# Kernel tuning notes

Measured on AMD Instinct MI355X. Metric: run time of the kernel, lower is better.

## Reference

```python
import jax, jax.numpy as jnp
import numpy as np

D_MODEL = 1024
D_HIDDEN = 4096
NUM_EXPERTS = 8
TOP_K = 2
B, S = 2, 2048


def setup_inputs() -> dict:
    key = jax.random.key(0)
    ks = jax.random.split(key, 9)
    sc = 0.02
    x = jax.random.normal(ks[0], (B, S, D_MODEL), dtype=jnp.float32)
    w1 = jax.random.normal(ks[1], (NUM_EXPERTS, D_MODEL, D_HIDDEN), dtype=jnp.float32) * sc
    b1 = jnp.zeros((NUM_EXPERTS, D_HIDDEN), dtype=jnp.float32)
    w2 = jax.random.normal(ks[2], (NUM_EXPERTS, D_MODEL, D_HIDDEN), dtype=jnp.float32) * sc
    b2 = jnp.zeros((NUM_EXPERTS, D_HIDDEN), dtype=jnp.float32)
    wo = jax.random.normal(ks[3], (NUM_EXPERTS, D_HIDDEN, D_MODEL), dtype=jnp.float32) * sc
    bo = jnp.zeros((NUM_EXPERTS, D_MODEL), dtype=jnp.float32)
    router_w = jax.random.normal(ks[4], (D_MODEL, NUM_EXPERTS), dtype=jnp.float32) * sc
    router_b = jnp.zeros((NUM_EXPERTS,), dtype=jnp.float32)
    return {"x": x, "router_w": router_w, "router_b": router_b,
            "w1": w1, "b1": b1, "w2": w2, "b2": b2, "wo": wo, "bo": bo}


def reference(x, router_w, router_b, w1, b1, w2, b2, wo, bo):
    b, s, d = x.shape
    E = w1.shape[0]
    xf = x.reshape(-1, d)                               # [T, d]
    logits = xf @ router_w + router_b                   # [T, E]
    probs = jax.nn.softmax(logits, axis=-1)
    topk_p, topk_i = jax.lax.top_k(probs, TOP_K)        # [T, K]
    onehot = jax.nn.one_hot(topk_i, E, dtype=probs.dtype)  # [T, K, E]
    combine = (onehot * topk_p[..., None]).sum(axis=1)  # [T, E] per-token expert weight
    out = jnp.zeros_like(xf)
    for e in range(E):  # fixed small expert loop; weight is 0 for unselected tokens
        h = (xf @ w1[e] + b1[e]) * jax.nn.silu(xf @ w2[e] + b2[e])  # [T, H]
        out = out + combine[:, e:e + 1] * (h @ wo[e] + bo[e])
    # load-balancing loss: fraction of tokens routed to each expert x mean prob
    f_i = (onehot.sum(axis=1) > 0).astype(probs.dtype).mean(axis=0)  # [E]
    P_i = probs.mean(axis=0)                                          # [E]
    lb_loss = 0.01 * E * jnp.sum(f_i * P_i)
    return out.reshape(b, s, d), lb_loss
```

## Files before the change

kernel.cpp:

```cpp
#include <hip/hip_runtime.h>
#include <hip/hip_bf16.h>
#include <stdint.h>


#define T_TOKENS 4096
#define DM 1024
#define DH 4096
#define N_EXP 8
#define N_PAIRS (T_TOKENS * 2)
#define MAX_TILES 96

typedef __hip_bfloat16 bf16_t;
typedef __bf16 bf16x8 __attribute__((ext_vector_type(8)));
typedef float  f32x4  __attribute__((ext_vector_type(4)));
typedef unsigned short ushort4v __attribute__((ext_vector_type(4)));

#define WS_COUNTS   0
#define WS_OFFSETS  32
#define WS_PSUM     96
#define WS_NTILES   128
#define WS_CURSOR   192
#define WS_TILE_E   256
#define WS_TILE_M0  768
#define WS_E_OF     4096
#define WS_W_OF     69632
#define WS_TOK_OF   102400
#define WS_WT_OF    135168
#define WS_SLOT_OF  167936
#define WS_HBUF     (1u<<20)
#define WS_YPAIR    (WS_HBUF + (size_t)N_PAIRS*DH*2)
#define WS_NEEDED   (WS_YPAIR + (size_t)N_PAIRS*DM*2)
#define WS_XBF      WS_NEEDED
#define WS_W1T      (WS_XBF + (size_t)T_TOKENS*DM*2)
#define WS_W2T      (WS_W1T + (size_t)N_EXP*DM*DH*2)
#define WS_WOT      (WS_W2T + (size_t)N_EXP*DM*DH*2)
#define WS_NEEDED_BIG (WS_WOT + (size_t)N_EXP*DM*DH*2)

#define PITCH 40

__device__ __forceinline__ unsigned short f2bf(float f) {
  bf16_t h = __float2bfloat16(f);
  return *(unsigned short*)&h;
}

__device__ __forceinline__ void gload16(const void* g, void* l) {
  __builtin_amdgcn_global_load_lds(
      (const __attribute__((address_space(1))) unsigned int*)g,
      (__attribute__((address_space(3))) unsigned int*)l, 16, 0, 0);
}

#define RT_BLOCKS 64
#define RT_TPB (T_TOKENS / RT_BLOCKS)
#define RT_TPW (RT_TPB / 4)

__global__ __launch_bounds__(256) void k_router(const float* __restrict__ x,
                                                const float* __restrict__ rw,
                                                const float* __restrict__ rb,
                                                char* __restrict__ ws) {
  __shared__ float s_psum[4][8];
  __shared__ unsigned long long s_hist[4];
  int tid = threadIdx.x, lane = tid & 63, wave = tid >> 6;
  int t0 = blockIdx.x * RT_TPB + wave * RT_TPW;
  int* e_of = (int*)(ws + WS_E_OF);
  float* w_of = (float*)(ws + WS_W_OF);

  float lpsum[8];
#pragma unroll
  for (int e = 0; e < 8; ++e) lpsum[e] = 0.f;
  unsigned long long lhist = 0ull;

  for (int tt = 0; tt < RT_TPW; ++tt) {
    int t = t0 + tt;
    float acc[8];
#pragma unroll
    for (int e = 0; e < 8; ++e) acc[e] = 0.f;
    const float* xr = x + (size_t)t * DM;
    for (int j = lane; j < DM; j += 64) {
      float xv = xr[j];
      float4 r01 = *(const float4*)(rw + j * 8);
      float4 r23 = *(const float4*)(rw + j * 8 + 4);
      acc[0] += xv * r01.x; acc[1] += xv * r01.y;
      acc[2] += xv * r01.z; acc[3] += xv * r01.w;
      acc[4] += xv * r23.x; acc[5] += xv * r23.y;
      acc[6] += xv * r23.z; acc[7] += xv * r23.w;
    }
#pragma unroll
    for (int m = 1; m < 64; m <<= 1) {
#pragma unroll
      for (int e = 0; e < 8; ++e) acc[e] += __shfl_xor(acc[e], m);
    }
    float mx = -1e30f;
#pragma unroll
    for (int e = 0; e < 8; ++e) { acc[e] += rb[e]; mx = fmaxf(mx, acc[e]); }
    float s = 0.f;
#pragma unroll
    for (int e = 0; e < 8; ++e) { acc[e] = __expf(acc[e] - mx); s += acc[e]; }
    float inv = 1.f / s;
#pragma unroll
    for (int e = 0; e < 8; ++e) { acc[e] *= inv; lpsum[e] += acc[e]; }
    int i1 = 0;
#pragma unroll
    for (int e = 1; e < 8; ++e) if (acc[e] > acc[i1]) i1 = e;
    int i2 = -1;
#pragma unroll
    for (int e = 0; e < 8; ++e) if (e != i1 && (i2 < 0 || acc[e] > acc[i2])) i2 = e;
    lhist += (1ull << (i1 * 8)) + (1ull << (i2 * 8));
    if (lane == 0) {
      e_of[2 * t] = i1; e_of[2 * t + 1] = i2;
      w_of[2 * t] = acc[i1]; w_of[2 * t + 1] = acc[i2];
    }
  }
  if (lane == 0) {
#pragma unroll
    for (int e = 0; e < 8; ++e) s_psum[wave][e] = lpsum[e];
    s_hist[wave] = lhist;
  }
  __syncthreads();
  if (tid < 8) {
    float p = s_psum[0][tid] + s_psum[1][tid] + s_psum[2][tid] + s_psum[3][tid];
    atomicAdd((float*)(ws + WS_PSUM) + tid, p);
    int c = 0;
#pragma unroll
    for (int w = 0; w < 4; ++w) c += (int)((s_hist[w] >> (tid * 8)) & 0xff);
    atomicAdd((int*)(ws + WS_COUNTS) + tid, c);
  }
}

__global__ void k_scan(char* __restrict__ ws, float* __restrict__ out) {
  if (threadIdx.x == 0 && blockIdx.x == 0) {
    int* counts = (int*)(ws + WS_COUNTS);
    int* offs = (int*)(ws + WS_OFFSETS);
    int* te = (int*)(ws + WS_TILE_E);
    int* tm = (int*)(ws + WS_TILE_M0);
    int off = 0, nt = 0;
    for (int e = 0; e < 8; ++e) {
      offs[e] = off;
      for (int m0 = 0; m0 < counts[e]; m0 += 128) { te[nt] = e; tm[nt] = off + m0; ++nt; }
      off += counts[e];
    }
    *(int*)(ws + WS_NTILES) = nt;
    float* psum = (float*)(ws + WS_PSUM);
    float lb = 0.f;
    for (int e = 0; e < 8; ++e)
      lb += ((float)counts[e] / (float)T_TOKENS) * (psum[e] / (float)T_TOKENS);
    lb *= 0.01f * 8.f;
    out[(size_t)T_TOKENS * DM] = lb;
  }
}

__global__ __launch_bounds__(256) void k_fill(char* __restrict__ ws) {
  __shared__ int hist[8];
  __shared__ int base[8];
  int tid = threadIdx.x;
  int i = blockIdx.x * 256 + tid;
  if (tid < 8) hist[tid] = 0;
  __syncthreads();
  int e = ((const int*)(ws + WS_E_OF))[i];
  int rank = atomicAdd(&hist[e], 1);
  __syncthreads();
  if (tid < 8) base[tid] = atomicAdd((int*)(ws + WS_CURSOR) + tid, hist[tid]);
  __syncthreads();
  int slot = ((const int*)(ws + WS_OFFSETS))[e] + base[e] + rank;
  ((int*)(ws + WS_TOK_OF))[slot] = i >> 1;
  ((float*)(ws + WS_WT_OF))[slot] = ((const float*)(ws + WS_W_OF))[i];
  ((int*)(ws + WS_SLOT_OF))[i] = slot;
}

__global__ __launch_bounds__(256) void k_cvt_x(const float* __restrict__ x,
                                               char* __restrict__ ws) {
  int i = blockIdx.x * 256 + threadIdx.x;
  const float* s = x + (size_t)i * 8;
  float4 a = *(const float4*)s;
  float4 b = *(const float4*)(s + 4);
  uint4 v;
  v.x = (unsigned)f2bf(a.x) | ((unsigned)f2bf(a.y) << 16);
  v.y = (unsigned)f2bf(a.z) | ((unsigned)f2bf(a.w) << 16);
  v.z = (unsigned)f2bf(b.x) | ((unsigned)f2bf(b.y) << 16);
  v.w = (unsigned)f2bf(b.z) | ((unsigned)f2bf(b.w) << 16);
  *(uint4*)(ws + WS_XBF + (size_t)i * 16) = v;
}

__global__ __launch_bounds__(256) void k_transp(const float* __restrict__ in,
                                                char* __restrict__ outc,
                                                int K, int N) {
  __shared__ __align__(16) float tile[64][68];
  int e = blockIdx.z;
  int k0 = blockIdx.y * 64, n0 = blockIdx.x * 64;
  int tid = threadIdx.x;
  const float* src = in + ((size_t)e * K + k0) * N + n0;
  int row = tid >> 2, c4 = (tid & 3) * 16;
#pragma unroll
  for (int j = 0; j < 4; ++j)
    *(float4*)&tile[row][c4 + j * 4] = *(const float4*)(src + (size_t)row * N + c4 + j * 4);
  __syncthreads();
  int n = tid >> 2, kc = (tid & 3) * 16;
  unsigned int pk[8];
#pragma unroll
  for (int j = 0; j < 8; ++j) {
    unsigned int lo = f2bf(tile[kc + 2 * j][n]);
    unsigned int hi = f2bf(tile[kc + 2 * j + 1][n]);
    pk[j] = lo | (hi << 16);
  }
  char* dst = outc + ((size_t)e * K * N + (size_t)(n0 + n) * K + k0 + kc) * 2;
  uint4 v0 = {pk[0], pk[1], pk[2], pk[3]};
  uint4 v1 = {pk[4], pk[5], pk[6], pk[7]};
  *(uint4*)dst = v0;
  *(uint4*)(dst + 16) = v1;
}

__global__ __launch_bounds__(256, 2) void k_gemm1_bf(const float* __restrict__ b1,
                                                     const float* __restrict__ b2,
                                                     char* __restrict__ ws) {
  __shared__ __align__(16) unsigned short As[128 * 64];
  __shared__ __align__(16) unsigned short Bs1[64 * 64];
  __shared__ __align__(16) unsigned short Bs2[64 * 64];
  __shared__ int tokLds[128];
  int tid = threadIdx.x;
  int tileIdx = blockIdx.y;
  if (tileIdx >= *(const int*)(ws + WS_NTILES)) return;
  int e = ((const int*)(ws + WS_TILE_E))[tileIdx];
  int m_start = ((const int*)(ws + WS_TILE_M0))[tileIdx];
  int m_end = ((const int*)(ws + WS_OFFSETS))[e] + ((const int*)(ws + WS_COUNTS))[e];
  int m_cnt = min(128, m_end - m_start);
  int n0 = blockIdx.x * 64;
  if (tid < 128) tokLds[tid] = ((const int*)(ws + WS_TOK_OF))[m_start + min(tid, m_cnt - 1)];
  __syncthreads();

  int lane = tid & 63, wave = tid >> 6;
  int wm = wave >> 1, wn = wave & 1;
  int lr = lane & 15, quad = lane >> 4;
  int lsub = lane >> 3;
  int clog = (lane & 7) ^ lsub;

  const char* xbf = ws + WS_XBF;
  const char* w1t = ws + WS_W1T + (size_t)e * DM * DH * 2;
  const char* w2t = ws + WS_W2T + (size_t)e * DM * DH * 2;

  const char* srcA[4];
#pragma unroll
  for (int i = 0; i < 4; ++i) {
    int r = (wave * 4 + i) * 8 + lsub;
    srcA[i] = xbf + (size_t)tokLds[r] * (DM * 2) + clog * 16;
  }
  const char* srcB1[2];
  const char* srcB2[2];
#pragma unroll
  for (int i = 0; i < 2; ++i) {
    int r = (wave * 2 + i) * 8 + lsub;
    srcB1[i] = w1t + (size_t)(n0 + r) * (DM * 2) + clog * 16;
    srcB2[i] = w2t + (size_t)(n0 + r) * (DM * 2) + clog * 16;
  }

  f32x4 acc1[4][2], acc2[4][2];
  f32x4 z = {0.f, 0.f, 0.f, 0.f};
#pragma unroll
  for (int i = 0; i < 4; ++i)
#pragma unroll
    for (int j = 0; j < 2; ++j) { acc1[i][j] = z; acc2[i][j] = z; }

  for (int kt = 0; kt < DM / 64; ++kt) {
    int kb = kt * 128;
#pragma unroll
    for (int i = 0; i < 4; ++i)
      gload16(srcA[i] + kb, &As[(wave * 4 + i) * 512]);
#pragma unroll
    for (int i = 0; i < 2; ++i) {
      gload16(srcB1[i] + kb, &Bs1[(wave * 2 + i) * 512]);
      gload16(srcB2[i] + kb, &Bs2[(wave * 2 + i) * 512]);
    }
    __syncthreads();
#pragma unroll
    for (int s = 0; s < 2; ++s) {
      int sw = (((s * 4 + quad) ^ (lr & 7)) << 3);
      bf16x8 a[4], f1[2], f2v[2];
#pragma unroll
      for (int mt = 0; mt < 4; ++mt)
        a[mt] = *(const bf16x8*)&As[(wm * 64 + mt * 16 + lr) * 64 + sw];
#pragma unroll
      for (int nt = 0; nt < 2; ++nt) {
        int off = (wn * 32 + nt * 16 + lr) * 64 + sw;
        f1[nt]  = *(const bf16x8*)&Bs1[off];
        f2v[nt] = *(const bf16x8*)&Bs2[off];
      }
#pragma unroll
      for (int mt = 0; mt < 4; ++mt)
#pragma unroll
        for (int nt = 0; nt < 2; ++nt) {
          acc1[mt][nt] = __builtin_amdgcn_mfma_f32_16x16x32_bf16(a[mt], f1[nt],  acc1[mt][nt], 0, 0, 0);
          acc2[mt][nt] = __builtin_amdgcn_mfma_f32_16x16x32_bf16(a[mt], f2v[nt], acc2[mt][nt], 0, 0, 0);
        }
    }
    __syncthreads();
  }
  bf16_t* Hbuf = (bf16_t*)(ws + WS_HBUF);
#pragma unroll
  for (int mt = 0; mt < 4; ++mt) {
    int growb = wm * 64 + mt * 16 + quad * 4;
#pragma unroll
    for (int nt = 0; nt < 2; ++nt) {
      int col = n0 + wn * 32 + nt * 16 + lr;
      float b1v = b1[e * DH + col];
      float b2v = b2[e * DH + col];
#pragma unroll
      for (int r = 0; r < 4; ++r) {
        int grow = growb + r;
        if (grow < m_cnt) {
          float v1 = acc1[mt][nt][r] + b1v;
          float v2 = acc2[mt][nt][r] + b2v;
          float hh = v1 * (v2 / (1.f + __expf(-v2)));
          Hbuf[(size_t)(m_start + grow) * DH + col] = __float2bfloat16(hh);
        }
      }
    }
  }
}

__global__ __launch_bounds__(256, 2) void k_gemm2_bf(const float* __restrict__ bo,
                                                     char* __restrict__ ws) {
  __shared__ __align__(16) unsigned short As[128 * 64];
  __shared__ __align__(16) unsigned short Bs[128 * 64];
  int tid = threadIdx.x;
  int tileIdx = blockIdx.y;
  if (tileIdx >= *(const int*)(ws + WS_NTILES)) return;
  int e = ((const int*)(ws + WS_TILE_E))[tileIdx];
  int m_start = ((const int*)(ws + WS_TILE_M0))[tileIdx];
  int m_end = ((const int*)(ws + WS_OFFSETS))[e] + ((const int*)(ws + WS_COUNTS))[e];
  int m_cnt = min(128, m_end - m_start);
  int n0 = blockIdx.x * 128;

  int lane = tid & 63, wave = tid >> 6;
  int wm = wave >> 1, wn = wave & 1;
  int lr = lane & 15, quad = lane >> 4;
  int lsub = lane >> 3;
  int clog = (lane & 7) ^ lsub;

  const char* hb = ws + WS_HBUF;
  const char* wot = ws + WS_WOT + (size_t)e * DM * DH * 2;

  const char* srcA[4];
  const char* srcB[4];
#pragma unroll
  for (int i = 0; i < 4; ++i) {
    int r = (wave * 4 + i) * 8 + lsub;
    int hrow = m_start + min(r, m_cnt - 1);
    srcA[i] = hb + (size_t)hrow * (DH * 2) + clog * 16;
    srcB[i] = wot + (size_t)(n0 + r) * (DH * 2) + clog * 16;
  }

  f32x4 acc[4][4];
  f32x4 z = {0.f, 0.f, 0.f, 0.f};
#pragma unroll
  for (int i = 0; i < 4; ++i)
#pragma unroll
    for (int j = 0; j < 4; ++j) acc[i][j] = z;

  for (int kt = 0; kt < DH / 64; ++kt) {
    int kb = kt * 128;
#pragma unroll
    for (int i = 0; i < 4; ++i) {
      gload16(srcA[i] + kb, &As[(wave * 4 + i) * 512]);
      gload16(srcB[i] + kb, &Bs[(wave * 4 + i) * 512]);
    }
    __syncthreads();
#pragma unroll
    for (int s = 0; s < 2; ++s) {
      int sw = (((s * 4 + quad) ^ (lr & 7)) << 3);
      bf16x8 a[4], b[4];
#pragma unroll
      for (int mt = 0; mt < 4; ++mt)
        a[mt] = *(const bf16x8*)&As[(wm * 64 + mt * 16 + lr) * 64 + sw];
#pragma unroll
      for (int nt = 0; nt < 4; ++nt)
        b[nt] = *(const bf16x8*)&Bs[(wn * 64 + nt * 16 + lr) * 64 + sw];
#pragma unroll
      for (int mt = 0; mt < 4; ++mt)
#pragma unroll
        for (int nt = 0; nt < 4; ++nt)
          acc[mt][nt] = __builtin_amdgcn_mfma_f32_16x16x32_bf16(a[mt], b[nt], acc[mt][nt], 0, 0, 0);
    }
    __syncthreads();
  }
  bf16_t* Ypair = (bf16_t*)(ws + WS_YPAIR);
  const float* wts = (const float*)(ws + WS_WT_OF);
#pragma unroll
  for (int mt = 0; mt < 4; ++mt) {
    int growb = wm * 64 + mt * 16 + quad * 4;
#pragma unroll
    for (int nt = 0; nt < 4; ++nt) {
      int col = n0 + wn * 64 + nt * 16 + lr;
      float bov = bo[e * DM + col];
#pragma unroll
      for (int r = 0; r < 4; ++r) {
        int grow = growb + r;
        if (grow < m_cnt) {
          int slot = m_start + grow;
          Ypair[(size_t)slot * DM + col] = __float2bfloat16((acc[mt][nt][r] + bov) * wts[slot]);
        }
      }
    }
  }
}

__global__ __launch_bounds__(256, 2) void k_gemm1(const float* __restrict__ x,
                                                  const float* __restrict__ w1,
                                                  const float* __restrict__ b1,
                                                  const float* __restrict__ w2,
                                                  const float* __restrict__ b2,
                                                  char* __restrict__ ws) {
  __shared__ __align__(16) unsigned short As[128 * PITCH];
  __shared__ __align__(16) unsigned short Bs1[64 * PITCH];
  __shared__ __align__(16) unsigned short Bs2[64 * PITCH];
  __shared__ int tokLds[128];
  int tid = threadIdx.x;
  int tileIdx = blockIdx.y;
  if (tileIdx >= *(const int*)(ws + WS_NTILES)) return;
  int e = ((const int*)(ws + WS_TILE_E))[tileIdx];
  int m_start = ((const int*)(ws + WS_TILE_M0))[tileIdx];
  int m_end = ((const int*)(ws + WS_OFFSETS))[e] + ((const int*)(ws + WS_COUNTS))[e];
  int m_cnt = min(128, m_end - m_start);
  int n0 = blockIdx.x * 64;
  if (tid < 128) tokLds[tid] = ((const int*)(ws + WS_TOK_OF))[m_start + min(tid, m_cnt - 1)];
  __syncthreads();

  f32x4 acc1[4][2], acc2[4][2];
  f32x4 z = {0.f, 0.f, 0.f, 0.f};
#pragma unroll
  for (int i = 0; i < 4; ++i)
#pragma unroll
    for (int j = 0; j < 2; ++j) { acc1[i][j] = z; acc2[i][j] = z; }

  int lane = tid & 63, wave = tid >> 6;
  int wm = wave >> 1, wn = wave & 1;
  int lr = lane & 15, quad = lane >> 4;
  int q = tid & 127, mat = tid >> 7;
  int pk = (q & 15) * 2, pn = (q >> 4) * 8;
  const float* Wm = mat ? w2 : w1;
  unsigned short* BsM = mat ? Bs2 : Bs1;
  const float* bBase = Wm + ((size_t)e * DM + pk) * DH + n0 + pn;

  int aRow[4], aKc[4];
  const float* aPtr[4];
#pragma unroll
  for (int h = 0; h < 4; ++h) {
    int c = tid + h * 256;
    aRow[h] = c >> 3; aKc[h] = (c & 7) * 4;
    aPtr[h] = x + (size_t)tokLds[aRow[h]] * DM + aKc[h];
  }

  float4 aR[4], bR[4];
#define G1_LOAD(k0)                                                  \
  {                                                                  \
    _Pragma("unroll")                                                \
    for (int h = 0; h < 4; ++h) aR[h] = *(const float4*)(aPtr[h] + (k0)); \
    const float* src = bBase + (size_t)(k0) * DH;                    \
    bR[0] = *(const float4*)src;                                     \
    bR[1] = *(const float4*)(src + 4);                               \
    bR[2] = *(const float4*)(src + DH);                              \
    bR[3] = *(const float4*)(src + DH + 4);                          \
  }

  G1_LOAD(0);
  for (int kt = 0; kt < DM / 32; ++kt) {
    __syncthreads();
#pragma unroll
    for (int h = 0; h < 4; ++h) {
      ushort4v wv = { f2bf(aR[h].x), f2bf(aR[h].y), f2bf(aR[h].z), f2bf(aR[h].w) };
      *(ushort4v*)&As[aRow[h] * PITCH + aKc[h]] = wv;
    }
    {
      float av[8] = {bR[0].x, bR[0].y, bR[0].z, bR[0].w, bR[1].x, bR[1].y, bR[1].z, bR[1].w};
      float bv[8] = {bR[2].x, bR[2].y, bR[2].z, bR[2].w, bR[3].x, bR[3].y, bR[3].z, bR[3].w};
#pragma unroll
      for (int j = 0; j < 8; ++j) {
        unsigned int wv = (unsigned int)f2bf(av[j]) | ((unsigned int)f2bf(bv[j]) << 16);
        *(unsigned int*)&BsM[(pn + j) * PITCH + pk] = wv;
      }
    }
    __syncthreads();
    if (kt + 1 < DM / 32) G1_LOAD((kt + 1) * 32);
    bf16x8 a[4], f1[2], f2v[2];
#pragma unroll
    for (int mt = 0; mt < 4; ++mt)
      a[mt] = *(const bf16x8*)&As[(wm * 64 + mt * 16 + lr) * PITCH + quad * 8];
#pragma unroll
    for (int nt = 0; nt < 2; ++nt) {
      f1[nt]  = *(const bf16x8*)&Bs1[(wn * 32 + nt * 16 + lr) * PITCH + quad * 8];
      f2v[nt] = *(const bf16x8*)&Bs2[(wn * 32 + nt * 16 + lr) * PITCH + quad * 8];
    }
#pragma unroll
    for (int mt = 0; mt < 4; ++mt)
#pragma unroll
      for (int nt = 0; nt < 2; ++nt) {
        acc1[mt][nt] = __builtin_amdgcn_mfma_f32_16x16x32_bf16(a[mt], f1[nt],  acc1[mt][nt], 0, 0, 0);
        acc2[mt][nt] = __builtin_amdgcn_mfma_f32_16x16x32_bf16(a[mt], f2v[nt], acc2[mt][nt], 0, 0, 0);
      }
  }
  bf16_t* Hbuf = (bf16_t*)(ws + WS_HBUF);
#pragma unroll
  for (int mt = 0; mt < 4; ++mt) {
    int growb = wm * 64 + mt * 16 + quad * 4;
#pragma unroll
    for (int nt = 0; nt < 2; ++nt) {
      int col = n0 + wn * 32 + nt * 16 + lr;
      float b1v = b1[e * DH + col];
      float b2v = b2[e * DH + col];
#pragma unroll
      for (int r = 0; r < 4; ++r) {
        int grow = growb + r;
        if (grow < m_cnt) {
          float v1 = acc1[mt][nt][r] + b1v;
          float v2 = acc2[mt][nt][r] + b2v;
          float hh = v1 * (v2 / (1.f + __expf(-v2)));
          Hbuf[(size_t)(m_start + grow) * DH + col] = __float2bfloat16(hh);
        }
      }
    }
  }
}

__global__ __launch_bounds__(256, 2) void k_gemm2(const float* __restrict__ wo,
                                                  const float* __restrict__ bo,
                                                  char* __restrict__ ws) {
  __shared__ __align__(16) unsigned short As[128 * PITCH];
  __shared__ __align__(16) unsigned short Bs[128 * PITCH];
  int tid = threadIdx.x;
  int tileIdx = blockIdx.y;
  if (tileIdx >= *(const int*)(ws + WS_NTILES)) return;
  int e = ((const int*)(ws + WS_TILE_E))[tileIdx];
  int m_start = ((const int*)(ws + WS_TILE_M0))[tileIdx];
  int m_end = ((const int*)(ws + WS_OFFSETS))[e] + ((const int*)(ws + WS_COUNTS))[e];
  int m_cnt = min(128, m_end - m_start);
  int n0 = blockIdx.x * 128;
  const bf16_t* Hbuf = (const bf16_t*)(ws + WS_HBUF);

  f32x4 acc[4][4];
  f32x4 z = {0.f, 0.f, 0.f, 0.f};
#pragma unroll
  for (int i = 0; i < 4; ++i)
#pragma unroll
    for (int j = 0; j < 4; ++j) acc[i][j] = z;

  int lane = tid & 63, wave = tid >> 6;
  int wm = wave >> 1, wn = wave & 1;
  int lr = lane & 15, quad = lane >> 4;
  int pk = (tid & 15) * 2, pn = (tid >> 4) * 8;
  const float* bBase = wo + ((size_t)e * DH + pk) * DM + n0 + pn;

  int aRow[2], aKc[2];
  const bf16_t* aPtr[2];
#pragma unroll
  for (int h = 0; h < 2; ++h) {
    int c = tid + h * 256;
    aRow[h] = c >> 2; aKc[h] = (c & 3) * 8;
    int hrow = m_start + min(aRow[h], m_cnt - 1);
    aPtr[h] = Hbuf + (size_t)hrow * DH + aKc[h];
  }

  int4 aR[2]; float4 bR[4];
#define G2_LOAD(k0)                                                  \
  {                                                                  \
    _Pragma("unroll")                                                \
    for (int h = 0; h < 2; ++h) aR[h] = *(const int4*)(aPtr[h] + (k0)); \
    const float* src = bBase + (size_t)(k0) * DM;                    \
    bR[0] = *(const float4*)src;                                     \
    bR[1] = *(const float4*)(src + 4);                               \
    bR[2] = *(const float4*)(src + DM);                              \
    bR[3] = *(const float4*)(src + DM + 4);                          \
  }

  G2_LOAD(0);
  for (int kt = 0; kt < DH / 32; ++kt) {
    __syncthreads();
#pragma unroll
    for (int h = 0; h < 2; ++h)
      *(int4*)&As[aRow[h] * PITCH + aKc[h]] = aR[h];
    {
      float av[8] = {bR[0].x, bR[0].y, bR[0].z, bR[0].w, bR[1].x, bR[1].y, bR[1].z, bR[1].w};
      float bv[8] = {bR[2].x, bR[2].y, bR[2].z, bR[2].w, bR[3].x, bR[3].y, bR[3].z, bR[3].w};
#pragma unroll
      for (int j = 0; j < 8; ++j) {
        unsigned int wv = (unsigned int)f2bf(av[j]) | ((unsigned int)f2bf(bv[j]) << 16);
        *(unsigned int*)&Bs[(pn + j) * PITCH + pk] = wv;
      }
    }
    __syncthreads();
    if (kt + 1 < DH / 32) G2_LOAD((kt + 1) * 32);
    bf16x8 a[4], b[4];
#pragma unroll
    for (int mt = 0; mt < 4; ++mt)
      a[mt] = *(const bf16x8*)&As[(wm * 64 + mt * 16 + lr) * PITCH + quad * 8];
#pragma unroll
    for (int nt = 0; nt < 4; ++nt)
      b[nt] = *(const bf16x8*)&Bs[(wn * 64 + nt * 16 + lr) * PITCH + quad * 8];
#pragma unroll
    for (int mt = 0; mt < 4; ++mt)
#pragma unroll
      for (int nt = 0; nt < 4; ++nt)
        acc[mt][nt] = __builtin_amdgcn_mfma_f32_16x16x32_bf16(a[mt], b[nt], acc[mt][nt], 0, 0, 0);
  }
  bf16_t* Ypair = (bf16_t*)(ws + WS_YPAIR);
  const float* wts = (const float*)(ws + WS_WT_OF);
#pragma unroll
  for (int mt = 0; mt < 4; ++mt) {
    int growb = wm * 64 + mt * 16 + quad * 4;
#pragma unroll
    for (int nt = 0; nt < 4; ++nt) {
      int col = n0 + wn * 64 + nt * 16 + lr;
      float bov = bo[e * DM + col];
#pragma unroll
      for (int r = 0; r < 4; ++r) {
        int grow = growb + r;
        if (grow < m_cnt) {
          int slot = m_start + grow;
          Ypair[(size_t)slot * DM + col] = __float2bfloat16((acc[mt][nt][r] + bov) * wts[slot]);
        }
      }
    }
  }
}

__global__ __launch_bounds__(256) void k_combine(const char* __restrict__ ws,
                                                 float* __restrict__ out) {
  int idx = blockIdx.x * 256 + threadIdx.x;
  int t = idx >> 7, c = (idx & 127) * 8;
  const int* slot_of = (const int*)(ws + WS_SLOT_OF);
  int s0 = slot_of[2 * t], s1 = slot_of[2 * t + 1];
  const unsigned short* Y = (const unsigned short*)(ws + WS_YPAIR);
  int4 ya = *(const int4*)(Y + (size_t)s0 * DM + c);
  int4 yb = *(const int4*)(Y + (size_t)s1 * DM + c);
  const unsigned short* pa = (const unsigned short*)&ya;
  const unsigned short* pb = (const unsigned short*)&yb;
  float res[8];
#pragma unroll
  for (int j = 0; j < 8; ++j) {
    res[j] = __uint_as_float((unsigned int)pa[j] << 16) +
             __uint_as_float((unsigned int)pb[j] << 16);
  }
  float4 o0 = {res[0], res[1], res[2], res[3]};
  float4 o1 = {res[4], res[5], res[6], res[7]};
  *(float4*)(out + (size_t)t * DM + c) = o0;
  *(float4*)(out + (size_t)t * DM + c + 4) = o1;
}

extern "C" void kernel_launch(void* const* d_in, const int* in_sizes, int n_in,
                              void* d_out, int out_size, void* d_ws, size_t ws_size,
                              hipStream_t stream) {
  const float* x  = (const float*)d_in[0];
  const float* rw = (const float*)d_in[1];
  const float* rb = (const float*)d_in[2];
  const float* w1 = (const float*)d_in[3];
  const float* b1 = (const float*)d_in[4];
  const float* w2 = (const float*)d_in[5];
  const float* b2 = (const float*)d_in[6];
  const float* wo = (const float*)d_in[7];
  const float* bo = (const float*)d_in[8];
  float* out = (float*)d_out;
  char* ws = (char*)d_ws;
  if (ws_size < WS_NEEDED) return;
  int big = ws_size >= WS_NEEDED_BIG;

  hipMemsetAsync(d_ws, 0, 4096, stream);
  k_router<<<RT_BLOCKS, 256, 0, stream>>>(x, rw, rb, ws);
  k_scan<<<1, 64, 0, stream>>>(ws, out);
  k_fill<<<N_PAIRS / 256, 256, 0, stream>>>(ws);
  if (big) {
    k_cvt_x<<<(T_TOKENS * DM / 8) / 256, 256, 0, stream>>>(x, ws);
    k_transp<<<dim3(DH / 64, DM / 64, N_EXP), 256, 0, stream>>>(w1, ws + WS_W1T, DM, DH);
    k_transp<<<dim3(DH / 64, DM / 64, N_EXP), 256, 0, stream>>>(w2, ws + WS_W2T, DM, DH);
    k_transp<<<dim3(DM / 64, DH / 64, N_EXP), 256, 0, stream>>>(wo, ws + WS_WOT, DH, DM);
    k_gemm1_bf<<<dim3(DH / 64, MAX_TILES), 256, 0, stream>>>(b1, b2, ws);
    k_gemm2_bf<<<dim3(DM / 128, MAX_TILES), 256, 0, stream>>>(bo, ws);
  } else {
    k_gemm1<<<dim3(DH / 64, MAX_TILES), 256, 0, stream>>>(x, w1, b1, w2, b2, ws);
    k_gemm2<<<dim3(DM / 128, MAX_TILES), 256, 0, stream>>>(wo, bo, ws);
  }
  k_combine<<<(T_TOKENS * DM / 8) / 256, 256, 0, stream>>>(ws, out);
}
```

Measured before the change: 827.9 us.

## Double-buffer LDS tiles in expert GEMMs with K=32 steps, widen router grid

Both expert GEMM kernels now use two LDS buffers with a K-step of 32 and issue global-to-LDS loads for the next step before computing the current one. This halves the barriers per step and overlaps memory with MFMA work, but drops the XOR swizzle, so LDS bank conflicts may increase. The router launches more blocks for parallelism, and the transpose kernel uses a padded scalar-store tile.

```diff
diff --git a/kernel.cpp b/kernel.cpp
--- a/kernel.cpp
+++ b/kernel.cpp
@@ -49,7 +49,7 @@
       (__attribute__((address_space(3))) unsigned int*)l, 16, 0, 0);
 }
 
-#define RT_BLOCKS 64
+#define RT_BLOCKS 256
 #define RT_TPB (T_TOKENS / RT_BLOCKS)
 #define RT_TPW (RT_TPB / 4)
 
@@ -183,15 +183,23 @@
 __global__ __launch_bounds__(256) void k_transp(const float* __restrict__ in,
                                                 char* __restrict__ outc,
                                                 int K, int N) {
-  __shared__ __align__(16) float tile[64][68];
+  __shared__ float tile[64][65];
   int e = blockIdx.z;
   int k0 = blockIdx.y * 64, n0 = blockIdx.x * 64;
   int tid = threadIdx.x;
   const float* src = in + ((size_t)e * K + k0) * N + n0;
   int row = tid >> 2, c4 = (tid & 3) * 16;
+  float4 v[4];
 #pragma unroll
   for (int j = 0; j < 4; ++j)
-    *(float4*)&tile[row][c4 + j * 4] = *(const float4*)(src + (size_t)row * N + c4 + j * 4);
+    v[j] = *(const float4*)(src + (size_t)row * N + c4 + j * 4);
+#pragma unroll
+  for (int j = 0; j < 4; ++j) {
+    tile[row][c4 + 4 * j]     = v[j].x;
+    tile[row][c4 + 4 * j + 1] = v[j].y;
+    tile[row][c4 + 4 * j + 2] = v[j].z;
+    tile[row][c4 + 4 * j + 3] = v[j].w;
+  }
   __syncthreads();
   int n = tid >> 2, kc = (tid & 3) * 16;
   unsigned int pk[8];
@@ -208,12 +216,13 @@
   *(uint4*)(dst + 16) = v1;
 }
 
+#define G1_NT (DM / 32)
 __global__ __launch_bounds__(256, 2) void k_gemm1_bf(const float* __restrict__ b1,
                                                      const float* __restrict__ b2,
                                                      char* __restrict__ ws) {
-  __shared__ __align__(16) unsigned short As[128 * 64];
-  __shared__ __align__(16) unsigned short Bs1[64 * 64];
-  __shared__ __align__(16) unsigned short Bs2[64 * 64];
+  __shared__ __align__(16) unsigned short As[2][128 * 32];
+  __shared__ __align__(16) unsigned short Bs1[2][64 * 32];
+  __shared__ __align__(16) unsigned short Bs2[2][64 * 32];
   __shared__ int tokLds[128];
   int tid = threadIdx.x;
   int tileIdx = blockIdx.y;
@@ -229,27 +238,17 @@
   int lane = tid & 63, wave = tid >> 6;
   int wm = wave >> 1, wn = wave & 1;
   int lr = lane & 15, quad = lane >> 4;
-  int lsub = lane >> 3;
-  int clog = (lane & 7) ^ lsub;
+  int rsub = lane >> 2;
+  int kch = (lane & 3) * 16;
 
   const char* xbf = ws + WS_XBF;
   const char* w1t = ws + WS_W1T + (size_t)e * DM * DH * 2;
   const char* w2t = ws + WS_W2T + (size_t)e * DM * DH * 2;
 
-  const char* srcA[4];
-#pragma unroll
-  for (int i = 0; i < 4; ++i) {
-    int r = (wave * 4 + i) * 8 + lsub;
-    srcA[i] = xbf + (size_t)tokLds[r] * (DM * 2) + clog * 16;
-  }
-  const char* srcB1[2];
-  const char* srcB2[2];
-#pragma unroll
-  for (int i = 0; i < 2; ++i) {
-    int r = (wave * 2 + i) * 8 + lsub;
-    srcB1[i] = w1t + (size_t)(n0 + r) * (DM * 2) + clog * 16;
-    srcB2[i] = w2t + (size_t)(n0 + r) * (DM * 2) + clog * 16;
-  }
+  const char* srcA0 = xbf + (size_t)tokLds[wave * 32 + rsub] * (DM * 2) + kch;
+  const char* srcA1 = xbf + (size_t)tokLds[wave * 32 + 16 + rsub] * (DM * 2) + kch;
+  const char* srcB1 = w1t + (size_t)(n0 + wave * 16 + rsub) * (DM * 2) + kch;
+  const char* srcB2 = w2t + (size_t)(n0 + wave * 16 + rsub) * (DM * 2) + kch;
 
   f32x4 acc1[4][2], acc2[4][2];
   f32x4 z = {0.f, 0.f, 0.f, 0.f};
@@ -258,39 +257,39 @@
 #pragma unroll
     for (int j = 0; j < 2; ++j) { acc1[i][j] = z; acc2[i][j] = z; }
 
-  for (int kt = 0; kt < DM / 64; ++kt) {
-    int kb = kt * 128;
-#pragma unroll
-    for (int i = 0; i < 4; ++i)
-      gload16(srcA[i] + kb, &As[(wave * 4 + i) * 512]);
-#pragma unroll
-    for (int i = 0; i < 2; ++i) {
-      gload16(srcB1[i] + kb, &Bs1[(wave * 2 + i) * 512]);
-      gload16(srcB2[i] + kb, &Bs2[(wave * 2 + i) * 512]);
-    }
+  gload16(srcA0, &As[0][(wave * 32) * 32]);
+  gload16(srcA1, &As[0][(wave * 32 + 16) * 32]);
+  gload16(srcB1, &Bs1[0][(wave * 16) * 32]);
+  gload16(srcB2, &Bs2[0][(wave * 16) * 32]);
+  __syncthreads();
+
+  int p = 0;
+  for (int kt = 0; kt < G1_NT; ++kt) {
+    if (kt + 1 < G1_NT) {
+      int kb = (kt + 1) * 64;
+      gload16(srcA0 + kb, &As[p ^ 1][(wave * 32) * 32]);
+      gload16(srcA1 + kb, &As[p ^ 1][(wave * 32 + 16) * 32]);
+      gload16(srcB1 + kb, &Bs1[p ^ 1][(wave * 16) * 32]);
+      gload16(srcB2 + kb, &Bs2[p ^ 1][(wave * 16) * 32]);
+    }
+    bf16x8 a[4], f1[2], f2v[2];
+#pragma unroll
+    for (int mt = 0; mt < 4; ++mt)
+      a[mt] = *(const bf16x8*)&As[p][(wm * 64 + mt * 16 + lr) * 32 + quad * 8];
+#pragma unroll
+    for (int nt = 0; nt < 2; ++nt) {
+      f1[nt]  = *(const bf16x8*)&Bs1[p][(wn * 32 + nt * 16 + lr) * 32 + quad * 8];
+      f2v[nt] = *(const bf16x8*)&Bs2[p][(wn * 32 + nt * 16 + lr) * 32 + quad * 8];
+    }
+#pragma unroll
+    for (int mt = 0; mt < 4; ++mt)
+#pragma unroll
+      for (int nt = 0; nt < 2; ++nt) {
+        acc1[mt][nt] = __builtin_amdgcn_mfma_f32_16x16x32_bf16(a[mt], f1[nt],  acc1[mt][nt], 0, 0, 0);
+        acc2[mt][nt] = __builtin_amdgcn_mfma_f32_16x16x32_bf16(a[mt], f2v[nt], acc2[mt][nt], 0, 0, 0);
+      }
     __syncthreads();
-#pragma unroll
-    for (int s = 0; s < 2; ++s) {
-      int sw = (((s * 4 + quad) ^ (lr & 7)) << 3);
-      bf16x8 a[4], f1[2], f2v[2];
-#pragma unroll
-      for (int mt = 0; mt < 4; ++mt)
-        a[mt] = *(const bf16x8*)&As[(wm * 64 + mt * 16 + lr) * 64 + sw];
-#pragma unroll
-      for (int nt = 0; nt < 2; ++nt) {
-        int off = (wn * 32 + nt * 16 + lr) * 64 + sw;
-        f1[nt]  = *(const bf16x8*)&Bs1[off];
-        f2v[nt] = *(const bf16x8*)&Bs2[off];
-      }
-#pragma unroll
-      for (int mt = 0; mt < 4; ++mt)
-#pragma unroll
-        for (int nt = 0; nt < 2; ++nt) {
-          acc1[mt][nt] = __builtin_amdgcn_mfma_f32_16x16x32_bf16(a[mt], f1[nt],  acc1[mt][nt], 0, 0, 0);
-          acc2[mt][nt] = __builtin_amdgcn_mfma_f32_16x16x32_bf16(a[mt], f2v[nt], acc2[mt][nt], 0, 0, 0);
-        }
-    }
-    __syncthreads();
+    p ^= 1;
   }
   bf16_t* Hbuf = (bf16_t*)(ws + WS_HBUF);
 #pragma unroll
@@ -315,10 +314,11 @@
   }
 }
 
+#define G2_NT (DH / 32)
 __global__ __launch_bounds__(256, 2) void k_gemm2_bf(const float* __restrict__ bo,
                                                      char* __restrict__ ws) {
-  __shared__ __align__(16) unsigned short As[128 * 64];
-  __shared__ __align__(16) unsigned short Bs[128 * 64];
+  __shared__ __align__(16) unsigned short As[2][128 * 32];
+  __shared__ __align__(16) unsigned short Bs[2][128 * 32];
   int tid = threadIdx.x;
   int tileIdx = blockIdx.y;
   if (tileIdx >= *(const int*)(ws + WS_NTILES)) return;
@@ -331,21 +331,17 @@
   int lane = tid & 63, wave = tid >> 6;
   int wm = wave >> 1, wn = wave & 1;
   int lr = lane & 15, quad = lane >> 4;
-  int lsub = lane >> 3;
-  int clog = (lane & 7) ^ lsub;
+  int rsub = lane >> 2;
+  int kch = (lane & 3) * 16;
 
   const char* hb = ws + WS_HBUF;
   const char* wot = ws + WS_WOT + (size_t)e * DM * DH * 2;
 
-  const char* srcA[4];
-  const char* srcB[4];
-#pragma unroll
-  for (int i = 0; i < 4; ++i) {
-    int r = (wave * 4 + i) * 8 + lsub;
-    int hrow = m_start + min(r, m_cnt - 1);
-    srcA[i] = hb + (size_t)hrow * (DH * 2) + clog * 16;
-    srcB[i] = wot + (size_t)(n0 + r) * (DH * 2) + clog * 16;
-  }
+  int ra0 = wave * 32 + rsub, ra1 = wave * 32 + 16 + rsub;
+  const char* srcA0 = hb + (size_t)(m_start + min(ra0, m_cnt - 1)) * (DH * 2) + kch;
+  const char* srcA1 = hb + (size_t)(m_start + min(ra1, m_cnt - 1)) * (DH * 2) + kch;
+  const char* srcB0 = wot + (size_t)(n0 + ra0) * (DH * 2) + kch;
+  const char* srcB1 = wot + (size_t)(n0 + ra1) * (DH * 2) + kch;
 
   f32x4 acc[4][4];
   f32x4 z = {0.f, 0.f, 0.f, 0.f};
@@ -354,31 +350,35 @@
 #pragma unroll
     for (int j = 0; j < 4; ++j) acc[i][j] = z;
 
-  for (int kt = 0; kt < DH / 64; ++kt) {
-    int kb = kt * 128;
-#pragma unroll
-    for (int i = 0; i < 4; ++i) {
-      gload16(srcA[i] + kb, &As[(wave * 4 + i) * 512]);
-      gload16(srcB[i] + kb, &Bs[(wave * 4 + i) * 512]);
-    }
+  gload16(srcA0, &As[0][(wave * 32) * 32]);
+  gload16(srcA1, &As[0][(wave * 32 + 16) * 32]);
+  gload16(srcB0, &Bs[0][(wave * 32) * 32]);
+  gload16(srcB1, &Bs[0][(wave * 32 + 16) * 32]);
+  __syncthreads();
+
+  int p = 0;
+  for (int kt = 0; kt < G2_NT; ++kt) {
+    if (kt + 1 < G2_NT) {
+      int kb = (kt + 1) * 64;
+      gload16(srcA0 + kb, &As[p ^ 1][(wave * 32) * 32]);
+      gload16(srcA1 + kb, &As[p ^ 1][(wave * 32 + 16) * 32]);
+      gload16(srcB0 + kb, &Bs[p ^ 1][(wave * 32) * 32]);
+      gload16(srcB1 + kb, &Bs[p ^ 1][(wave * 32 + 16) * 32]);
+    }
+    bf16x8 a[4], b[4];
+#pragma unroll
+    for (int mt = 0; mt < 4; ++mt)
+      a[mt] = *(const bf16x8*)&As[p][(wm * 64 + mt * 16 + lr) * 32 + quad * 8];
+#pragma unroll
+    for (int nt = 0; nt < 4; ++nt)
+      b[nt] = *(const bf16x8*)&Bs[p][(wn * 64 + nt * 16 + lr) * 32 + quad * 8];
+#pragma unroll
+    for (int mt = 0; mt < 4; ++mt)
+#pragma unroll
+      for (int nt = 0; nt < 4; ++nt)
+        acc[mt][nt] = __builtin_amdgcn_mfma_f32_16x16x32_bf16(a[mt], b[nt], acc[mt][nt], 0, 0, 0);
     __syncthreads();
-#pragma unroll
-    for (int s = 0; s < 2; ++s) {
-      int sw = (((s * 4 + quad) ^ (lr & 7)) << 3);
-      bf16x8 a[4], b[4];
-#pragma unroll
-      for (int mt = 0; mt < 4; ++mt)
-        a[mt] = *(const bf16x8*)&As[(wm * 64 + mt * 16 + lr) * 64 + sw];
-#pragma unroll
-      for (int nt = 0; nt < 4; ++nt)
-        b[nt] = *(const bf16x8*)&Bs[(wn * 64 + nt * 16 + lr) * 64 + sw];
-#pragma unroll
-      for (int mt = 0; mt < 4; ++mt)
-#pragma unroll
-        for (int nt = 0; nt < 4; ++nt)
-          acc[mt][nt] = __builtin_amdgcn_mfma_f32_16x16x32_bf16(a[mt], b[nt], acc[mt][nt], 0, 0, 0);
-    }
-    __syncthreads();
+    p ^= 1;
   }
   bf16_t* Ypair = (bf16_t*)(ws + WS_YPAIR);
   const float* wts = (const float*)(ws + WS_WT_OF);
```

New measurement: 785.9 us. -5.1%, faster.
